# Performance work log

Measured on AMD Instinct MI355X. Metric: run time of the kernel, lower is better.

## Reference

```python
import jax, jax.numpy as jnp
import numpy as np

P = 16        # patch size
SIM = 0.3     # similarity threshold (forward default arg `sim`)
STY_STD = 1000.0


def patchify(imgs):
    # (N,3,H,W) -> (N, h*w, p*p*3)
    N, C, H, W = imgs.shape
    h, w = H // P, W // P
    x = imgs.reshape(N, C, h, P, w, P)
    x = jnp.einsum('nchpwq->nhwpqc', x)
    return x.reshape(N, h * w, P * P * C)


def setup_inputs() -> dict:
    key = jax.random.key(0)
    k1, k2, k3, k4 = jax.random.split(key, 4)
    N, L, D = 2, 196, 768
    x = jax.random.normal(k1, (N, L + 1, D), dtype=jnp.float32)
    imgs = jax.random.normal(k2, (N, 3, 224, 224), dtype=jnp.float32)
    # torch trunc_normal_(std=1000, a=-2, b=2) == truncated normal on [-2,2]
    learnable_sty = (jax.random.truncated_normal(
        k3, -2.0 / STY_STD, 2.0 / STY_STD, (N, L, L, 1), dtype=jnp.float32) * STY_STD)
    noise = jax.random.normal(k4, (N, L, L, 1), dtype=jnp.float32)
    return {"x": x, "imgs": imgs, "learnable_sty": learnable_sty, "noise": noise}


def reference(x, imgs, learnable_sty, noise):
    imgs = patchify(imgs)                                   # (N, L, 768)
    cls_tokens, x = x[:, :1], x[:, 1:]
    N, L, D = x.shape

    # per-patch normalization (torch.var default is unbiased -> ddof=1)
    mean = imgs.mean(axis=-1, keepdims=True)
    var = jnp.var(imgs, axis=-1, keepdims=True, ddof=1)
    imgs_n = (imgs - mean) / jnp.sqrt(var + 1e-6)
    nrm = jnp.linalg.norm(imgs_n, axis=-1)                  # (N, L)
    Sim = jnp.einsum('aik,ajk->aij', imgs_n, imgs_n) / (nrm[:, :, None] * nrm[:, None, :])

    M0 = jnp.triu((Sim > SIM).astype(jnp.float32))          # (N, L, L), binary
    rows = jnp.arange(L)

    def body(i, M):
        # original loop breaks when sum == N*L; we freeze M once that holds
        done = M.sum() == N * L
        mask = (M[:, i, :] == 0).astype(M.dtype)            # (N, L)
        # rows <= i unchanged (M*M == M for binary), rows > i masked
        upd = jnp.where(rows[None, :, None] > i, M * mask[:, None, :], M)
        return jnp.where(done, M, upd)

    M = jax.lax.fori_loop(0, L - 1, body, M0)

    # decompose: phase (con) keeps grad, amplitude (sty) is detached
    fft = jnp.fft.fftn(x, axes=(-1,))
    con, sty = jnp.angle(fft), jnp.abs(fft)
    sty_d = jax.lax.stop_gradient(sty)

    avg_sum = (M[..., None] * sty_d[:, None, :, :]).sum(axis=2)   # (N, L, D)
    sty_mask = (avg_sum > 0).astype(jnp.float32)                   # (N, L, D)
    num = M.sum(axis=2)[..., None]                                 # (N, L, 1)
    avg = avg_sum / jnp.clip(num, 1e-7, None)                      # (N, L, D)
    std = jnp.sqrt(
        (M[..., None] * (sty_d[:, None, :, :] - avg[:, :, None, :]) ** 2).sum(axis=2)
        / jnp.clip(num, 1e-7, None))                               # (N, L, D)

    sty_para = sty_mask[:, None, :, :] * learnable_sty             # (N, L, L, D)
    sty_para = sty_para / jnp.clip(sty_para.sum(axis=2, keepdims=True), 1e-7, None)
    various = noise * std[:, None, :, :] + avg[:, None, :, :]      # (N, L, L, D)
    sum_sty = (sty_para * various).sum(axis=2)                     # (N, L, D)

    # compose: ifft(amp * e^{i phase}), torch .float() keeps the real part
    out = jnp.real(jnp.fft.ifftn(sum_sty * jnp.exp(1j * con), axes=(-1,))).astype(jnp.float32)
    return jnp.concatenate((cls_tokens, out), axis=1)
```

## Files before the change

kernel.cpp:

```cpp
#include <hip/hip_runtime.h>
#include <math.h>

typedef unsigned long long u64;

#define NBATCH 2
#define LTOK 196
#define DDIM 768
#define NROWS (NBATCH*LTOK)
#define NLD (NBATCH*LTOK*DDIM)

#define PI_F 3.14159265358979323846f
#define S3 0.86602540378443864676f

#define RTILE 7
#define JCH 4
#define JLEN 49
#define NCOMB (NBATCH*28*3*JCH)
#define GRIDB NROWS
#define NGRP 7
#define GSZ 56

__device__ __forceinline__ float aldf(const float* p) {
  unsigned u = __hip_atomic_load((const unsigned*)p, __ATOMIC_RELAXED,
                                 __HIP_MEMORY_SCOPE_AGENT);
  return __uint_as_float(u);
}
__device__ __forceinline__ void astf(float* p, float v) {
  __hip_atomic_store((unsigned*)p, __float_as_uint(v), __ATOMIC_RELAXED,
                     __HIP_MEMORY_SCOPE_AGENT);
}
__device__ __forceinline__ u64 ald64(const u64* p) {
  return __hip_atomic_load(p, __ATOMIC_RELAXED, __HIP_MEMORY_SCOPE_AGENT);
}
__device__ __forceinline__ void ast64(u64* p, u64 v) {
  __hip_atomic_store(p, v, __ATOMIC_RELAXED, __HIP_MEMORY_SCOPE_AGENT);
}

union ShMem {
  struct { float re[768]; float im[768]; float2 tw[128]; } fft;
  struct { double rs[4]; double rq[4]; float mu; float sc; } pat;
  struct { float ui[768]; u64 mask[4]; int last; } sim;
  struct { u64 Ml[NROWS*4]; int red[4]; int done; } gr;
  struct { u64 mrow[4]; } st;
  struct { float lsr[RTILE][JLEN], lnr[RTILE][JLEN]; } cmb;
};

__device__ __forceinline__ void gbar(unsigned* bar, int slot) {
  __syncthreads();
  if (threadIdx.x == 0) {
    unsigned* root = bar + (size_t)(slot * 8) * 32;
    unsigned* grp  = bar + (size_t)(slot * 8 + 1 + (blockIdx.x / GSZ)) * 32;
    if (__hip_atomic_fetch_add(grp, 1u, __ATOMIC_RELAXED,
                               __HIP_MEMORY_SCOPE_AGENT) == GSZ - 1u) {
      __hip_atomic_fetch_add(root, 1u, __ATOMIC_RELAXED,
                             __HIP_MEMORY_SCOPE_AGENT);
    }
    while (__hip_atomic_load(root, __ATOMIC_RELAXED,
                             __HIP_MEMORY_SCOPE_AGENT) < (unsigned)NGRP) {
      __builtin_amdgcn_s_sleep(8);
    }
  }
  __syncthreads();
}

__device__ __forceinline__ void fft_butterfly(float* re, float* im,
                                              const float2* T,
                                              int tau, int s, int half) {
  int sub = tau >> 7;
  int b = tau & 127;
  int j = b & (half - 1);
  int p0 = (sub << 8) + ((b >> (s - 1)) << s) + j;
  int p1 = p0 + half;
  float2 w = T[j << (8 - s)];
  float xr = re[p1], xi = im[p1];
  float tr = w.x * xr - w.y * xi;
  float ti = w.x * xi + w.y * xr;
  float ur = re[p0], ui = im[p0];
  re[p0] = ur + tr; im[p0] = ui + ti;
  re[p1] = ur - tr; im[p1] = ui - ti;
}

__device__ __forceinline__ void fft_stages(float* re, float* im,
                                           const float2* T, int t) {
#pragma unroll
  for (int s = 1; s <= 8; s++) {
    int half = 1 << (s - 1);
    fft_butterfly(re, im, T, t, s, half);
    if (t < 128) fft_butterfly(re, im, T, t + 256, s, half);
    __syncthreads();
  }
}

__device__ void greedy_block(u64* __restrict__ Mb, ShMem& sh) {
  int t = threadIdx.x;
  for (int w = t; w < NROWS * 4; w += 256) sh.gr.Ml[w] = ald64(&Mb[w]);
  __syncthreads();
  for (int i = 0; i < LTOK - 1; i++) {
    int s = 0;
    for (int w = t; w < NROWS * 4; w += 256) s += __popcll(sh.gr.Ml[w]);
#pragma unroll
    for (int o = 32; o > 0; o >>= 1) s += __shfl_down(s, o);
    if ((t & 63) == 0) sh.gr.red[t >> 6] = s;
    __syncthreads();
    if (t == 0)
      sh.gr.done = ((sh.gr.red[0] + sh.gr.red[1] + sh.gr.red[2] + sh.gr.red[3]) == NROWS) ? 1 : 0;
    __syncthreads();
    if (sh.gr.done) break;
    for (int w = t; w < NROWS * 4; w += 256) {
      int a = w / (LTOK * 4);
      int rem = w - a * (LTOK * 4);
      int r = rem >> 2, wi = rem & 3;
      if (r > i) sh.gr.Ml[w] &= ~sh.gr.Ml[(a * LTOK + i) * 4 + wi];
    }
    __syncthreads();
  }
  for (int w = t; w < NROWS * 4; w += 256) ast64(&Mb[w], sh.gr.Ml[w]);
}

__global__ __launch_bounds__(256, 2) void mega(
    const float* __restrict__ imgs, const float* __restrict__ x,
    const float* __restrict__ ls, const float* __restrict__ nz,
    float* __restrict__ out,
    float* __restrict__ uT, float* __restrict__ sty,
    float* __restrict__ phre, float* __restrict__ phim,
    float* __restrict__ sstd, float* __restrict__ smsk,
    float* __restrict__ numP, float* __restrict__ denP,
    u64* __restrict__ Mb, unsigned* __restrict__ bar) {
  __shared__ ShMem sh;
  const int t = threadIdx.x;
  const int blk = blockIdx.x;
  const int a = blk / LTOK, i = blk - (blk / LTOK) * LTOK;
  unsigned* ctr = bar + 32 * 32;

  {
    int hh = i / 14, ww = i - hh * 14;
    float loc[3];
    double s = 0.0, sq = 0.0;
#pragma unroll
    for (int e = 0; e < 3; e++) {
      int d = t + (e << 8);
      int p = d / 48, r = d - p * 48;
      int q2 = r / 3, c = r - q2 * 3;
      float val = imgs[((size_t)(a * 3 + c) * 224 + (hh * 16 + p)) * 224 + (ww * 16 + q2)];
      loc[e] = val;
      s += (double)val;
      sq += (double)val * (double)val;
    }
#pragma unroll
    for (int o = 32; o > 0; o >>= 1) { s += __shfl_down(s, o); sq += __shfl_down(sq, o); }
    if ((t & 63) == 0) { sh.pat.rs[t >> 6] = s; sh.pat.rq[t >> 6] = sq; }
    __syncthreads();
    if (t == 0) {
      double S = sh.pat.rs[0] + sh.pat.rs[1] + sh.pat.rs[2] + sh.pat.rs[3];
      double Q = sh.pat.rq[0] + sh.pat.rq[1] + sh.pat.rq[2] + sh.pat.rq[3];
      double mean = S / 768.0;
      double ss = Q - S * S / 768.0;
      if (ss < 1e-30) ss = 1e-30;
      sh.pat.mu = (float)mean;
      sh.pat.sc = (float)(1.0 / sqrt(ss));
    }
    __syncthreads();
    float mu = sh.pat.mu, sc = sh.pat.sc;
    int col = a * LTOK + i;
#pragma unroll
    for (int e = 0; e < 3; e++) {
      int d = t + (e << 8);
      astf(&uT[(size_t)d * NROWS + col], (loc[e] - mu) * sc);
    }
  }
  __syncthreads();

  {
    if (t < 128) {
      float sn, cs;
      __sincosf(-2.0f * PI_F * (float)t / 256.0f, &sn, &cs);
      sh.fft.tw[t] = make_float2(cs, sn);
    }
    size_t row = ((size_t)a * (LTOK + 1) + 1 + i) * DDIM;
#pragma unroll
    for (int e = 0; e < 3; e++) {
      int d = t + (e << 8);
      int m = d / 3, r = d - 3 * m;
      int p = (r << 8) + (__brev((unsigned)m) >> 24);
      sh.fft.re[p] = x[row + d];
      sh.fft.im[p] = 0.f;
    }
    __syncthreads();
    fft_stages(sh.fft.re, sh.fft.im, sh.fft.tw, t);
    float a0r = sh.fft.re[t],       a0i = sh.fft.im[t];
    float a1r = sh.fft.re[256 + t], a1i = sh.fft.im[256 + t];
    float a2r = sh.fft.re[512 + t], a2i = sh.fft.im[512 + t];
    float sn, cs;
    __sincosf(-2.0f * PI_F * (float)t / 768.0f, &sn, &cs);
    float2 w1 = make_float2(cs, sn);
    float2 w2 = make_float2(cs * cs - sn * sn, 2.f * cs * sn);
    float b1r = a1r * w1.x - a1i * w1.y, b1i = a1r * w1.y + a1i * w1.x;
    float b2r = a2r * w2.x - a2i * w2.y, b2i = a2r * w2.y + a2i * w2.x;
    float Xr[3], Xi[3];
    Xr[0] = a0r + b1r + b2r;
    Xi[0] = a0i + b1i + b2i;
    Xr[1] = a0r + (-0.5f * b1r + S3 * b1i) + (-0.5f * b2r - S3 * b2i);
    Xi[1] = a0i + (-0.5f * b1i - S3 * b1r) + (-0.5f * b2i + S3 * b2r);
    Xr[2] = a0r + (-0.5f * b1r - S3 * b1i) + (-0.5f * b2r + S3 * b2i);
    Xi[2] = a0i + (-0.5f * b1i + S3 * b1r) + (-0.5f * b2i - S3 * b2r);
    size_t ob = ((size_t)a * LTOK + i) * DDIM + t;
#pragma unroll
    for (int s2 = 0; s2 < 3; s2++) {
      float mag = sqrtf(Xr[s2] * Xr[s2] + Xi[s2] * Xi[s2]);
      size_t o = ob + (s2 << 8);
      astf(&sty[o], mag);
      if (mag > 0.f) { astf(&phre[o], Xr[s2] / mag); astf(&phim[o], Xi[s2] / mag); }
      else           { astf(&phre[o], 1.f);          astf(&phim[o], 0.f);          }
    }
  }
  gbar(bar, 0);

  {
    if (t < 4) sh.sim.mask[t] = 0ull;
    int coli = a * LTOK + i;
#pragma unroll
    for (int e = 0; e < 3; e++) {
      int d = t + (e << 8);
      sh.sim.ui[d] = aldf(&uT[(size_t)d * NROWS + coli]);
    }
    __syncthreads();
    int j = i + t;
    if (j < LTOK) {
      const float* col = uT + (a * LTOK + j);
      float acc[8];
#pragma unroll
      for (int k = 0; k < 8; k++) acc[k] = 0.f;
      for (int d = 0; d < 768; d += 8) {
#pragma unroll
        for (int k = 0; k < 8; k++)
          acc[k] += sh.sim.ui[d + k] * aldf(col + (size_t)(d + k) * NROWS);
      }
      float dot = ((acc[0] + acc[1]) + (acc[2] + acc[3])) +
                  ((acc[4] + acc[5]) + (acc[6] + acc[7]));
      if (dot > 0.3f) atomicOr(&sh.sim.mask[j >> 6], 1ull << (j & 63));
    }
    __syncthreads();
    if (t < 4) ast64(&Mb[((size_t)a * LTOK + i) * 4 + t], sh.sim.mask[t]);
    __syncthreads();
    if (t == 0)
      sh.sim.last = (__hip_atomic_fetch_add(ctr, 1u, __ATOMIC_RELAXED,
                                            __HIP_MEMORY_SCOPE_AGENT) == GRIDB - 1u) ? 1 : 0;
    __syncthreads();
    int amlast = sh.sim.last;
    __syncthreads();
    if (amlast) greedy_block(Mb, sh);
  }
  gbar(bar, 1);

  {
    float* savg = uT;
    if (t < 4) sh.st.mrow[t] = ald64(&Mb[((size_t)a * LTOK + i) * 4 + t]);
    __syncthreads();
    int num = __popcll(sh.st.mrow[0]) + __popcll(sh.st.mrow[1]) +
              __popcll(sh.st.mrow[2]) + __popcll(sh.st.mrow[3]);
    float fnum = fmaxf((float)num, 1e-7f);
    float acc0 = 0.f, acc1 = 0.f, acc2 = 0.f;
    for (int w = 0; w < 4; w++) {
      u64 m = sh.st.mrow[w];
      while (m) {
        int b = __ffsll(m) - 1; m &= (m - 1);
        int jj = (w << 6) + b;
        const float* sr = sty + ((size_t)a * LTOK + jj) * DDIM;
        acc0 += aldf(&sr[t]); acc1 += aldf(&sr[t + 256]); acc2 += aldf(&sr[t + 512]);
      }
    }
    float av0 = acc0 / fnum, av1 = acc1 / fnum, av2 = acc2 / fnum;
    float sq0 = 0.f, sq1 = 0.f, sq2 = 0.f;
    for (int w = 0; w < 4; w++) {
      u64 m = sh.st.mrow[w];
      while (m) {
        int b = __ffsll(m) - 1; m &= (m - 1);
        int jj = (w << 6) + b;
        const float* sr = sty + ((size_t)a * LTOK + jj) * DDIM;
        float e0 = aldf(&sr[t]) - av0, e1 = aldf(&sr[t + 256]) - av1, e2 = aldf(&sr[t + 512]) - av2;
        sq0 += e0 * e0; sq1 += e1 * e1; sq2 += e2 * e2;
      }
    }
    size_t o = ((size_t)a * LTOK + i) * DDIM + t;
    float mk0 = acc0 > 0.f ? 1.f : 0.f;
    float mk1 = acc1 > 0.f ? 1.f : 0.f;
    float mk2 = acc2 > 0.f ? 1.f : 0.f;
    astf(&smsk[o], mk0);           astf(&smsk[o + 256], mk1);           astf(&smsk[o + 512], mk2);
    astf(&savg[o], mk0 * av0);     astf(&savg[o + 256], mk1 * av1);     astf(&savg[o + 512], mk2 * av2);
    astf(&sstd[o], mk0 * sqrtf(sq0 / fnum));
    astf(&sstd[o + 256], mk1 * sqrtf(sq1 / fnum));
    astf(&sstd[o + 512], mk2 * sqrtf(sq2 / fnum));
  }
  gbar(bar, 2);

  {
    const float* savg = uT;
    for (int u = blk; u < NCOMB; u += GRIDB) {
      int ea = u / 336;
      int rem = u - ea * 336;
      int it = rem / 12;
      int r2 = rem - it * 12;
      int dc = r2 >> 2;
      int jc = r2 & 3;
      int i0 = it * RTILE;
      int j0 = jc * JLEN;
      int d = (dc << 8) + t;
      __syncthreads();
      for (int idx = t; idx < RTILE * JLEN; idx += 256) {
        int ii = idx / JLEN, j = idx - ii * JLEN;
        size_t o = ((size_t)(ea * LTOK + i0 + ii)) * LTOK + j0 + j;
        float l = ls[o];
        sh.cmb.lsr[ii][j] = l;
        sh.cmb.lnr[ii][j] = l * nz[o];
      }
      __syncthreads();
      float nm[RTILE], dn[RTILE];
#pragma unroll
      for (int ii = 0; ii < RTILE; ii++) { nm[ii] = 0.f; dn[ii] = 0.f; }
#pragma unroll 7
      for (int j = 0; j < JLEN; j++) {
        size_t b = ((size_t)(ea * LTOK + j0 + j)) * DDIM + d;
        float sd = aldf(&sstd[b]), sv = aldf(&savg[b]), sm = aldf(&smsk[b]);
#pragma unroll
        for (int ii = 0; ii < RTILE; ii++) {
          nm[ii] += sh.cmb.lnr[ii][j] * sd;
          nm[ii] += sh.cmb.lsr[ii][j] * sv;
          dn[ii] += sh.cmb.lsr[ii][j] * sm;
        }
      }
#pragma unroll
      for (int ii = 0; ii < RTILE; ii++) {
        size_t o = ((size_t)jc * NROWS + (ea * LTOK + i0 + ii)) * DDIM + d;
        astf(&numP[o], nm[ii]);
        astf(&denP[o], dn[ii]);
      }
    }
  }
  gbar(bar, 3);

  {
    if (blk < NBATCH) {
      size_t b = (size_t)blk * (LTOK + 1) * DDIM;
      out[b + t] = x[b + t];
      out[b + t + 256] = x[b + t + 256];
      out[b + t + 512] = x[b + t + 512];
    }
    if (t < 128) {
      float sn, cs;
      __sincosf(2.0f * PI_F * (float)t / 256.0f, &sn, &cs);
      sh.fft.tw[t] = make_float2(cs, sn);
    }
    size_t rowz = ((size_t)a * LTOK + i) * DDIM;
#pragma unroll
    for (int e = 0; e < 3; e++) {
      int d = t + (e << 8);
      float num = 0.f, den = 0.f;
#pragma unroll
      for (int jc = 0; jc < JCH; jc++) {
        size_t o = (size_t)jc * NROWS * DDIM + rowz + d;
        num += aldf(&numP[o]);
        den += aldf(&denP[o]);
      }
      float mg = num / fmaxf(den, 1e-7f);
      int m = d / 3, r = d - 3 * m;
      int p = (r << 8) + (__brev((unsigned)m) >> 24);
      sh.fft.re[p] = mg * aldf(&phre[rowz + d]);
      sh.fft.im[p] = mg * aldf(&phim[rowz + d]);
    }
    __syncthreads();
    fft_stages(sh.fft.re, sh.fft.im, sh.fft.tw, t);
    float a0r = sh.fft.re[t],       a0i = sh.fft.im[t];
    float a1r = sh.fft.re[256 + t], a1i = sh.fft.im[256 + t];
    float a2r = sh.fft.re[512 + t], a2i = sh.fft.im[512 + t];
    float sn, cs;
    __sincosf(2.0f * PI_F * (float)t / 768.0f, &sn, &cs);
    float2 w1 = make_float2(cs, sn);
    float2 w2 = make_float2(cs * cs - sn * sn, 2.f * cs * sn);
    float b1r = a1r * w1.x - a1i * w1.y, b1i = a1r * w1.y + a1i * w1.x;
    float b2r = a2r * w2.x - a2i * w2.y, b2i = a2r * w2.y + a2i * w2.x;
    float Xr[3];
    Xr[0] = a0r + b1r + b2r;
    Xr[1] = a0r + (-0.5f * b1r - S3 * b1i) + (-0.5f * b2r + S3 * b2i);
    Xr[2] = a0r + (-0.5f * b1r + S3 * b1i) + (-0.5f * b2r - S3 * b2i);
    size_t ob = ((size_t)a * (LTOK + 1) + 1 + i) * DDIM + t;
    const float inv = 1.0f / 768.0f;
    out[ob]       = Xr[0] * inv;
    out[ob + 256] = Xr[1] * inv;
    out[ob + 512] = Xr[2] * inv;
  }
}

extern "C" void kernel_launch(void* const* d_in, const int* in_sizes, int n_in,
                              void* d_out, int out_size, void* d_ws, size_t ws_size,
                              hipStream_t stream) {
  (void)in_sizes; (void)n_in; (void)out_size; (void)ws_size;
  const float* x    = (const float*)d_in[0];
  const float* imgs = (const float*)d_in[1];
  const float* ls   = (const float*)d_in[2];
  const float* nz   = (const float*)d_in[3];
  float* out = (float*)d_out;

  float* wf   = (float*)d_ws;
  float* uT   = wf;
  float* sty  = wf + (size_t)NLD;
  float* phre = wf + 2 * (size_t)NLD;
  float* phim = wf + 3 * (size_t)NLD;
  float* sstd = wf + 4 * (size_t)NLD;
  float* smsk = wf + 5 * (size_t)NLD;
  float* numP = wf + 6 * (size_t)NLD;
  float* denP = wf + 10 * (size_t)NLD;
  u64* Mb = (u64*)(wf + 14 * (size_t)NLD);
  unsigned* bar = (unsigned*)(Mb + (size_t)NROWS * 4);

  hipMemsetAsync((void*)bar, 0, 33 * 128, stream);

  mega<<<GRIDB, 256, 0, stream>>>(imgs, x, ls, nz, out,
                                  uT, sty, phre, phim, sstd, smsk,
                                  numP, denP, Mb, bar);
}
```

Baseline: 135.7 us.

## Batch similarity rows per block and enlarge combine row tile

The similarity phase now has each of 50 blocks compute eight query rows at once. Each column value loaded from global memory is reused across eight accumulators, where before every block recomputed a single row and reloaded all columns. The combine phase doubles its row tile to 14, so each block handles exactly one work unit with no loop and reuses each sstd/savg/smsk load across more rows. The cost is that fewer blocks are active in these phases, so parallelism drops and per-block latency and register pressure rise.

New measurement: 147.3 us. +8.6%, slower.

```diff
diff --git a/kernel.cpp b/kernel.cpp
--- a/kernel.cpp
+++ b/kernel.cpp
@@ -12,13 +12,17 @@
 #define PI_F 3.14159265358979323846f
 #define S3 0.86602540378443864676f
 
-#define RTILE 7
+#define RTILE 14
 #define JCH 4
 #define JLEN 49
-#define NCOMB (NBATCH*28*3*JCH)
+#define NCOMB (NBATCH*14*3*JCH)
 #define GRIDB NROWS
 #define NGRP 7
 #define GSZ 56
+
+#define SGRP 8
+#define NSIMG 25
+#define NSIMB (NBATCH*NSIMG)
 
 __device__ __forceinline__ float aldf(const float* p) {
   unsigned u = __hip_atomic_load((const unsigned*)p, __ATOMIC_RELAXED,
@@ -39,7 +43,7 @@
 union ShMem {
   struct { float re[768]; float im[768]; float2 tw[128]; } fft;
   struct { double rs[4]; double rq[4]; float mu; float sc; } pat;
-  struct { float ui[768]; u64 mask[4]; int last; } sim;
+  struct { float simT[768][SGRP]; u64 gmask[SGRP][4]; int last; } sim2;
   struct { u64 Ml[NROWS*4]; int red[4]; int done; } gr;
   struct { u64 mrow[4]; } st;
   struct { float lsr[RTILE][JLEN], lnr[RTILE][JLEN]; } cmb;
@@ -215,38 +219,53 @@
   }
   gbar(bar, 0);
 
-  {
-    if (t < 4) sh.sim.mask[t] = 0ull;
-    int coli = a * LTOK + i;
-#pragma unroll
-    for (int e = 0; e < 3; e++) {
-      int d = t + (e << 8);
-      sh.sim.ui[d] = aldf(&uT[(size_t)d * NROWS + coli]);
-    }
-    __syncthreads();
-    int j = i + t;
+  if (blk < NSIMB) {
+    int sa = blk / NSIMG, grp = blk - sa * NSIMG;
+    int i0 = grp * SGRP;
+    int nrow = (LTOK - i0 < SGRP) ? (LTOK - i0) : SGRP;
+    int base = sa * LTOK + i0;
+    for (int idx = t; idx < SGRP * 4; idx += 256) ((u64*)sh.sim2.gmask)[idx] = 0ull;
+    for (int idx = t; idx < 768 * SGRP; idx += 256) {
+      int d = idx >> 3, r = idx & 7;
+      sh.sim2.simT[d][r] = (r < nrow) ? aldf(&uT[(size_t)d * NROWS + base + r]) : 0.f;
+    }
+    __syncthreads();
+    int j = i0 + t;
     if (j < LTOK) {
-      const float* col = uT + (a * LTOK + j);
-      float acc[8];
-#pragma unroll
-      for (int k = 0; k < 8; k++) acc[k] = 0.f;
-      for (int d = 0; d < 768; d += 8) {
-#pragma unroll
-        for (int k = 0; k < 8; k++)
-          acc[k] += sh.sim.ui[d + k] * aldf(col + (size_t)(d + k) * NROWS);
-      }
-      float dot = ((acc[0] + acc[1]) + (acc[2] + acc[3])) +
-                  ((acc[4] + acc[5]) + (acc[6] + acc[7]));
-      if (dot > 0.3f) atomicOr(&sh.sim.mask[j >> 6], 1ull << (j & 63));
-    }
-    __syncthreads();
-    if (t < 4) ast64(&Mb[((size_t)a * LTOK + i) * 4 + t], sh.sim.mask[t]);
+      const float* colp = uT + sa * LTOK + j;
+      float acc[SGRP];
+#pragma unroll
+      for (int k = 0; k < SGRP; k++) acc[k] = 0.f;
+      for (int d0 = 0; d0 < 768; d0 += 16) {
+        float cv[16];
+#pragma unroll
+        for (int q = 0; q < 16; q++) cv[q] = aldf(colp + (size_t)(d0 + q) * NROWS);
+#pragma unroll
+        for (int q = 0; q < 16; q++) {
+          float4 A0 = *(const float4*)&sh.sim2.simT[d0 + q][0];
+          float4 A1 = *(const float4*)&sh.sim2.simT[d0 + q][4];
+          acc[0] += A0.x * cv[q]; acc[1] += A0.y * cv[q];
+          acc[2] += A0.z * cv[q]; acc[3] += A0.w * cv[q];
+          acc[4] += A1.x * cv[q]; acc[5] += A1.y * cv[q];
+          acc[6] += A1.z * cv[q]; acc[7] += A1.w * cv[q];
+        }
+      }
+#pragma unroll
+      for (int k = 0; k < SGRP; k++) {
+        int ii = i0 + k;
+        if (k < nrow && j >= ii && acc[k] > 0.3f)
+          atomicOr(&sh.sim2.gmask[k][j >> 6], 1ull << (j & 63));
+      }
+    }
+    __syncthreads();
+    if (t < nrow * 4)
+      ast64(&Mb[((size_t)(base + (t >> 2))) * 4 + (t & 3)], sh.sim2.gmask[t >> 2][t & 3]);
     __syncthreads();
     if (t == 0)
-      sh.sim.last = (__hip_atomic_fetch_add(ctr, 1u, __ATOMIC_RELAXED,
-                                            __HIP_MEMORY_SCOPE_AGENT) == GRIDB - 1u) ? 1 : 0;
-    __syncthreads();
-    int amlast = sh.sim.last;
+      sh.sim2.last = (__hip_atomic_fetch_add(ctr, 1u, __ATOMIC_RELAXED,
+                                             __HIP_MEMORY_SCOPE_AGENT) == NSIMB - 1u) ? 1 : 0;
+    __syncthreads();
+    int amlast = sh.sim2.last;
     __syncthreads();
     if (amlast) greedy_block(Mb, sh);
   }
@@ -293,47 +312,44 @@
   }
   gbar(bar, 2);
 
-  {
+  if (blk < NCOMB) {
     const float* savg = uT;
-    for (int u = blk; u < NCOMB; u += GRIDB) {
-      int ea = u / 336;
-      int rem = u - ea * 336;
-      int it = rem / 12;
-      int r2 = rem - it * 12;
-      int dc = r2 >> 2;
-      int jc = r2 & 3;
-      int i0 = it * RTILE;
-      int j0 = jc * JLEN;
-      int d = (dc << 8) + t;
-      __syncthreads();
-      for (int idx = t; idx < RTILE * JLEN; idx += 256) {
-        int ii = idx / JLEN, j = idx - ii * JLEN;
-        size_t o = ((size_t)(ea * LTOK + i0 + ii)) * LTOK + j0 + j;
-        float l = ls[o];
-        sh.cmb.lsr[ii][j] = l;
-        sh.cmb.lnr[ii][j] = l * nz[o];
-      }
-      __syncthreads();
-      float nm[RTILE], dn[RTILE];
-#pragma unroll
-      for (int ii = 0; ii < RTILE; ii++) { nm[ii] = 0.f; dn[ii] = 0.f; }
+    int ea = blk / 168;
+    int rem = blk - ea * 168;
+    int it = rem / 12;
+    int r2 = rem - it * 12;
+    int dc = r2 >> 2;
+    int jc = r2 & 3;
+    int i0 = it * RTILE;
+    int j0 = jc * JLEN;
+    int d = (dc << 8) + t;
+    for (int idx = t; idx < RTILE * JLEN; idx += 256) {
+      int ii = idx / JLEN, j = idx - ii * JLEN;
+      size_t o = ((size_t)(ea * LTOK + i0 + ii)) * LTOK + j0 + j;
+      float l = ls[o];
+      sh.cmb.lsr[ii][j] = l;
+      sh.cmb.lnr[ii][j] = l * nz[o];
+    }
+    __syncthreads();
+    float nm[RTILE], dn[RTILE];
+#pragma unroll
+    for (int ii = 0; ii < RTILE; ii++) { nm[ii] = 0.f; dn[ii] = 0.f; }
 #pragma unroll 7
-      for (int j = 0; j < JLEN; j++) {
-        size_t b = ((size_t)(ea * LTOK + j0 + j)) * DDIM + d;
-        float sd = aldf(&sstd[b]), sv = aldf(&savg[b]), sm = aldf(&smsk[b]);
-#pragma unroll
-        for (int ii = 0; ii < RTILE; ii++) {
-          nm[ii] += sh.cmb.lnr[ii][j] * sd;
-          nm[ii] += sh.cmb.lsr[ii][j] * sv;
-          dn[ii] += sh.cmb.lsr[ii][j] * sm;
-        }
-      }
+    for (int j = 0; j < JLEN; j++) {
+      size_t b = ((size_t)(ea * LTOK + j0 + j)) * DDIM + d;
+      float sd = aldf(&sstd[b]), sv = aldf(&savg[b]), sm = aldf(&smsk[b]);
 #pragma unroll
       for (int ii = 0; ii < RTILE; ii++) {
-        size_t o = ((size_t)jc * NROWS + (ea * LTOK + i0 + ii)) * DDIM + d;
-        astf(&numP[o], nm[ii]);
-        astf(&denP[o], dn[ii]);
-      }
+        nm[ii] += sh.cmb.lnr[ii][j] * sd;
+        nm[ii] += sh.cmb.lsr[ii][j] * sv;
+        dn[ii] += sh.cmb.lsr[ii][j] * sm;
+      }
+    }
+#pragma unroll
+    for (int ii = 0; ii < RTILE; ii++) {
+      size_t o = ((size_t)jc * NROWS + (ea * LTOK + i0 + ii)) * DDIM + d;
+      astf(&numP[o], nm[ii]);
+      astf(&denP[o], dn[ii]);
     }
   }
   gbar(bar, 3);
```
